# Kernel optimization log

Measured on AMD Instinct MI355X. Metric: run time of the kernel, lower is better.

## Reference

```python
import jax, jax.numpy as jnp
import numpy as np

HIDDEN = 1024
N_HEADS = 16
HEAD_DIM = HIDDEN // N_HEADS  # 64
B, N = 2, 2048
SCALE = HIDDEN ** (-0.5)  # NOTE: original scales by full hidden_size, not head_dim


def setup_inputs() -> dict:
    key = jax.random.key(0)
    k1, k2 = jax.random.split(key)
    hidden_states = jax.random.normal(k1, (B, N, HIDDEN), dtype=jnp.float32)
    attention_mask = jnp.ones((B, N), dtype=jnp.int32)
    # per-head no-bias Linear(hidden -> 3*head_dim), stacked: [h, hidden, 3*head_dim]
    W_qkv = jax.random.normal(k2, (N_HEADS, HIDDEN, 3 * HEAD_DIM), dtype=jnp.float32) * (HIDDEN ** -0.5)
    return {"hidden_states": hidden_states, "attention_mask": attention_mask, "W_qkv": W_qkv}


def reference(hidden_states, attention_mask, W_qkv):
    # qkv: [b, h, n, 3*d]
    qkv = jnp.einsum('bnD,hDe->bhne', hidden_states, W_qkv)
    q, k, v = jnp.split(qkv, 3, axis=-1)  # each [b, h, n, d]
    scores = jnp.einsum('bhid,bhjd->bhij', q, k) * SCALE
    mask = attention_mask[:, None, None, :] == 0  # [b,1,1,n]
    scores = jnp.where(mask, -jnp.inf, scores)
    attn = jax.nn.softmax(scores, axis=-1)
    out = jnp.einsum('bhij,bhjd->bhid', attn, v)  # [b, h, n, d]
    # rearrange 'b h n d -> b n (h d)'
    return jnp.transpose(out, (0, 2, 1, 3)).reshape(out.shape[0], out.shape[2], -1)
```

## Files before the change

kernel.cpp:

```cpp
#include <hip/hip_runtime.h>
#include <hip/hip_bf16.h>


#define NH   16
#define HD   64
#define SEQ  2048
#define HID  1024
#define E3   192
#define QSCALE 0.04508422017f
#define MBIAS  -43.2808512f

typedef __attribute__((ext_vector_type(8))) short short8;
typedef __attribute__((ext_vector_type(4))) float f32x4;
typedef unsigned short ushort_t;

#define MFMA16(a, b, c) __builtin_amdgcn_mfma_f32_16x16x32_bf16((a), (b), (c), 0, 0, 0)

#if __has_builtin(__builtin_amdgcn_exp2f)
#define EXP2(x) __builtin_amdgcn_exp2f(x)
#else
#define EXP2(x) exp2f(x)
#endif

static __device__ __forceinline__ ushort_t f2bf(float x) {
    unsigned u = __builtin_bit_cast(unsigned, x);
    unsigned r = u + 0x7fff + ((u >> 16) & 1);
    return (ushort_t)(r >> 16);
}

static __device__ __forceinline__ unsigned pack_trunc(float hi, float lo) {
#if __has_builtin(__builtin_amdgcn_perm)
    return __builtin_amdgcn_perm(__builtin_bit_cast(unsigned, hi),
                                 __builtin_bit_cast(unsigned, lo), 0x07060302u);
#else
    return (__builtin_bit_cast(unsigned, hi) & 0xffff0000u) |
           (__builtin_bit_cast(unsigned, lo) >> 16);
#endif
}

static __device__ __forceinline__ void load_lds16(const void* g, void* l) {
    __builtin_amdgcn_global_load_lds(
        (__attribute__((address_space(1))) void*)(g),
        (__attribute__((address_space(3))) void*)(l), 16, 0, 0);
}

__global__ void k_detect(const unsigned* __restrict__ X32, int* __restrict__ flagp) {
    __shared__ int cnt;
    if (threadIdx.x == 0) cnt = 0;
    __syncthreads();
    int local = 0;
#pragma unroll
    for (int i = 0; i < 4; ++i) {
        unsigned u = X32[(size_t)(threadIdx.x * 4 + i) * 1973 + 7];
        int b = (u >> 7) & 0xFF;
        if (b >= 0x68 && b <= 0x90) ++local;
    }
    atomicAdd(&cnt, local);
    __syncthreads();
    if (threadIdx.x == 0) *flagp = (cnt < 512) ? 1 : 0;
}

__global__ __launch_bounds__(256) void k_cvt_x(const void* __restrict__ Xv,
                                               ushort_t* __restrict__ Xb,
                                               const int* __restrict__ flagp) {
    const int isf32 = *flagp;
    const size_t base = ((size_t)blockIdx.x * 256 + threadIdx.x) * 16;
    if (isf32) {
        const float* Xf = (const float*)Xv;
        ushort_t tmp[16];
#pragma unroll
        for (int c = 0; c < 4; ++c) {
            float4 v = *(const float4*)(Xf + base + c * 4);
            tmp[c * 4 + 0] = f2bf(v.x); tmp[c * 4 + 1] = f2bf(v.y);
            tmp[c * 4 + 2] = f2bf(v.z); tmp[c * 4 + 3] = f2bf(v.w);
        }
        *(float4*)(Xb + base)     = ((const float4*)tmp)[0];
        *(float4*)(Xb + base + 8) = ((const float4*)tmp)[1];
    } else {
        const ushort_t* Xh = (const ushort_t*)Xv;
        *(float4*)(Xb + base)     = *(const float4*)(Xh + base);
        *(float4*)(Xb + base + 8) = *(const float4*)(Xh + base + 8);
    }
}

__global__ __launch_bounds__(256) void k_cvt_w(const void* __restrict__ Wv,
                                               ushort_t* __restrict__ Wt,
                                               const int* __restrict__ flagp) {
    __shared__ ushort_t tile[64][72];
    const int isf32 = *flagp;
    const int h  = blockIdx.x;
    const int dt = blockIdx.y;
    const int et = blockIdx.z;
    const int D0 = dt * 64, e0 = et * 64;
    const int t  = threadIdx.x;
#pragma unroll
    for (int r = 0; r < 2; ++r) {
        int row = r * 32 + (t >> 3);
        int col = (t & 7) * 8;
        size_t base = ((size_t)(h * HID + D0 + row)) * E3 + e0 + col;
        if (isf32) {
            const float* Wf = (const float*)Wv;
            float4 a = *(const float4*)(Wf + base);
            float4 c = *(const float4*)(Wf + base + 4);
            tile[row][col + 0] = f2bf(a.x); tile[row][col + 1] = f2bf(a.y);
            tile[row][col + 2] = f2bf(a.z); tile[row][col + 3] = f2bf(a.w);
            tile[row][col + 4] = f2bf(c.x); tile[row][col + 5] = f2bf(c.y);
            tile[row][col + 6] = f2bf(c.z); tile[row][col + 7] = f2bf(c.w);
        } else {
            *(float4*)&tile[row][col] = *(const float4*)((const ushort_t*)Wv + base);
        }
    }
    __syncthreads();
#pragma unroll
    for (int r = 0; r < 2; ++r) {
        int erow = r * 32 + (t >> 3);
        int dcol = (t & 7) * 8;
        ushort_t vals[8];
#pragma unroll
        for (int i = 0; i < 8; ++i) vals[i] = tile[dcol + i][erow];
        *(float4*)(Wt + ((size_t)(h * E3 + e0 + erow)) * HID + D0 + dcol) = *(float4*)vals;
    }
}

__global__ __launch_bounds__(256) void k_qkv(const ushort_t* __restrict__ Xb,
                                             const ushort_t* __restrict__ Wt,
                                             ushort_t* __restrict__ Qb,
                                             ushort_t* __restrict__ Kb,
                                             ushort_t* __restrict__ Vtb) {
    __shared__ __align__(16) ushort_t smem[2 * 128 * 64];
    ushort_t* Xl = smem;
    ushort_t* Wl = smem + 128 * 64;

    const int e0 = blockIdx.x * 128;
    const int m0 = blockIdx.y * 128;
    const int b  = m0 >> 11;
    const int n0 = m0 & 2047;
    const int t = threadIdx.x;
    const int w = t >> 6, lane = t & 63, l15 = lane & 15, quad = lane >> 4;
    const int wrow0 = (w & 1) * 64, wcol0 = (w >> 1) * 64;
    const int srow = lane >> 3;
    const int scb  = (lane & 7) ^ srow;

    f32x4 acc[4][4];
#pragma unroll
    for (int i = 0; i < 4; ++i)
#pragma unroll
        for (int j = 0; j < 4; ++j) acc[i][j] = (f32x4){0.f, 0.f, 0.f, 0.f};

    for (int k0 = 0; k0 < HID; k0 += 64) {
        __syncthreads();
#pragma unroll
        for (int cc = 0; cc < 4; ++cc) {
            const int ch  = w * 4 + cc;
            const int row = ch * 8 + srow;
            load_lds16(Xb + (size_t)(m0 + row) * HID + k0 + scb * 8, &Xl[ch * 512]);
            load_lds16(Wt + (size_t)(e0 + row) * HID + k0 + scb * 8, &Wl[ch * 512]);
        }
        __syncthreads();
#pragma unroll
        for (int kh = 0; kh < 2; ++kh) {
            short8 af[4], bfm[4];
#pragma unroll
            for (int i = 0; i < 4; ++i) {
                const int r = wrow0 + i * 16 + l15;
                af[i] = *(const short8*)&Xl[r * 64 + ((kh * 4 + quad) ^ (r & 7)) * 8];
            }
#pragma unroll
            for (int j = 0; j < 4; ++j) {
                const int r = wcol0 + j * 16 + l15;
                bfm[j] = *(const short8*)&Wl[r * 64 + ((kh * 4 + quad) ^ (r & 7)) * 8];
            }
#pragma unroll
            for (int i = 0; i < 4; ++i)
#pragma unroll
                for (int j = 0; j < 4; ++j)
                    acc[i][j] = MFMA16(af[i], bfm[j], acc[i][j]);
        }
    }

    ushort_t* Vbuf = smem;
    __syncthreads();
#pragma unroll
    for (int i = 0; i < 4; ++i) {
#pragma unroll
        for (int j = 0; j < 4; ++j) {
            const int E0v = e0 + wcol0 + j * 16;
            const int hh  = E0v / 192;
            const int r0  = E0v - hh * 192;
            const int bh  = b * NH + hh;
            const int nb  = n0 + wrow0 + i * 16 + quad * 4;
            if (r0 < 64) {
                const int e = r0 + l15;
#pragma unroll
                for (int reg = 0; reg < 4; ++reg)
                    Qb[((size_t)bh * SEQ + nb + reg) * HD + e] = f2bf(acc[i][j][reg] * QSCALE);
            } else if (r0 < 128) {
                const int e = r0 - 64 + l15;
#pragma unroll
                for (int reg = 0; reg < 4; ++reg)
                    Kb[((size_t)bh * SEQ + nb + reg) * HD + e] = f2bf(acc[i][j][reg]);
            } else {
                const int d  = r0 - 128 + l15;
                const int nl = wrow0 + i * 16 + quad * 4;
#pragma unroll
                for (int reg = 0; reg < 4; ++reg)
                    Vbuf[d * 136 + nl + reg] = f2bf(acc[i][j][reg]);
            }
        }
    }
    const int m3 = blockIdx.x % 3;
    if (m3 != 0) {
        __syncthreads();
        const int hv  = (e0 + ((m3 == 1) ? 0 : 64)) / 192;
        const int bhv = b * NH + hv;
        const int dr = t >> 2, part = t & 3;
        size_t dst = ((size_t)bhv * HD + dr) * SEQ + n0 + part * 32;
#pragma unroll
        for (int c = 0; c < 4; ++c) {
            float4 v = *(const float4*)&Vbuf[dr * 136 + part * 32 + c * 8];
            *(float4*)(Vtb + dst + c * 8) = v;
        }
    }
}

__global__ __launch_bounds__(512) void k_attn(const ushort_t* __restrict__ Qb,
                                              const ushort_t* __restrict__ Kb,
                                              const ushort_t* __restrict__ Vtb,
                                              const int* __restrict__ mask,
                                              void* __restrict__ outv,
                                              const int* __restrict__ flagp) {
    __shared__ __align__(16) char smem_raw[59392];
    ushort_t* kvbuf = (ushort_t*)smem_raw;
    ushort_t* Pl    = (ushort_t*)(smem_raw + 32768);
    float*    biasl = (float*)(smem_raw + 51200);

    const int isf32 = *flagp;
    const int q0 = blockIdx.x * 128;
    const int bh = blockIdx.y;
    const int b  = bh >> 4, h = bh & 15;
    const int t  = threadIdx.x;
    const int w  = t >> 6, lane = t & 63, l15 = lane & 15, quad = lane >> 4;
    const int srow = lane >> 3;
    const int scb  = (lane & 7) ^ srow;

    const f32x4 zero4 = {0.f, 0.f, 0.f, 0.f};

    {
        ushort_t* kb = kvbuf;
        ushort_t* vb = kvbuf + 4096;
        const int row = w * 8 + srow;
        load_lds16(Kb  + ((size_t)bh * SEQ + row) * HD + scb * 8, &kb[w * 512]);
        load_lds16(Vtb + ((size_t)bh * HD + row) * SEQ + scb * 8, &vb[w * 512]);
    }

    int lm = 0;
    for (int i = t; i < SEQ; i += 512) {
        int mv = mask[b * SEQ + i];
        biasl[i] = mv ? 0.0f : MBIAS;
        lm |= (mv == 0);
    }
    const int use_bias = __syncthreads_or(lm);

    const int qrow = q0 + w * 16 + l15;
    short8 qa0 = *(const short8*)(Qb + ((size_t)bh * SEQ + qrow) * HD + quad * 8);
    short8 qa1 = *(const short8*)(Qb + ((size_t)bh * SEQ + qrow) * HD + 32 + quad * 8);

    f32x4 o[4];
#pragma unroll
    for (int mt = 0; mt < 4; ++mt) o[mt] = zero4;
    float l_r = 0.f;

    for (int j0 = 0; j0 < SEQ; j0 += 64) {
        const int cur = (j0 >> 6) & 1;
        __syncthreads();
        if (j0 + 64 < SEQ) {
            ushort_t* kb = kvbuf + (1 - cur) * 8192;
            ushort_t* vb = kb + 4096;
            const int row = w * 8 + srow;
            load_lds16(Kb  + ((size_t)bh * SEQ + j0 + 64 + row) * HD + scb * 8, &kb[w * 512]);
            load_lds16(Vtb + ((size_t)bh * HD + row) * SEQ + j0 + 64 + scb * 8, &vb[w * 512]);
        }
        ushort_t* kb = kvbuf + cur * 8192;
        ushort_t* vb = kb + 4096;

        f32x4 s[4];
#pragma unroll
        for (int jt = 0; jt < 4; ++jt) {
            const int rk = jt * 16 + l15;
            short8 kb0 = *(const short8*)&kb[rk * 64 + ((quad)     ^ (rk & 7)) * 8];
            short8 kb1 = *(const short8*)&kb[rk * 64 + ((4 + quad) ^ (rk & 7)) * 8];
            s[jt] = MFMA16(kb0, qa0, zero4);
            s[jt] = MFMA16(kb1, qa1, s[jt]);
        }
        if (use_bias) {
#pragma unroll
            for (int jt = 0; jt < 4; ++jt) {
                float4 bj = *(const float4*)&biasl[j0 + jt * 16 + quad * 4];
#pragma unroll
                for (int reg = 0; reg < 4; ++reg)
                    s[jt][reg] += ((const float*)&bj)[reg];
            }
        }

#pragma unroll
        for (int jt = 0; jt < 4; ++jt) {
            float p0 = EXP2(s[jt][0]);
            float p1 = EXP2(s[jt][1]);
            float p2 = EXP2(s[jt][2]);
            float p3 = EXP2(s[jt][3]);
            l_r += (p0 + p1) + (p2 + p3);
            uint2 u;
            u.x = pack_trunc(p1, p0);
            u.y = pack_trunc(p3, p2);
            *(uint2*)&Pl[(w * 16 + l15) * 72 + jt * 16 + quad * 4] = u;
        }
        short8 pb0 = *(const short8*)&Pl[(w * 16 + l15) * 72 + quad * 8];
        short8 pb1 = *(const short8*)&Pl[(w * 16 + l15) * 72 + 32 + quad * 8];
#pragma unroll
        for (int mt = 0; mt < 4; ++mt) {
            const int rv = mt * 16 + l15;
            short8 va0 = *(const short8*)&vb[rv * 64 + ((quad)     ^ (rv & 7)) * 8];
            short8 va1 = *(const short8*)&vb[rv * 64 + ((4 + quad) ^ (rv & 7)) * 8];
            o[mt] = MFMA16(va0, pb0, o[mt]);
            o[mt] = MFMA16(va1, pb1, o[mt]);
        }
    }

    l_r += __shfl_xor(l_r, 16);
    l_r += __shfl_xor(l_r, 32);
    const float rinv = 1.0f / l_r;

    __syncthreads();
    const int r = t >> 2, part = t & 3;
    if (!isf32) {
        ushort_t* Ol = (ushort_t*)smem_raw;
#pragma unroll
        for (int mt = 0; mt < 4; ++mt) {
            uint2 u;
            u.x = (unsigned)f2bf(o[mt][0] * rinv) | ((unsigned)f2bf(o[mt][1] * rinv) << 16);
            u.y = (unsigned)f2bf(o[mt][2] * rinv) | ((unsigned)f2bf(o[mt][3] * rinv) << 16);
            *(uint2*)&Ol[(w * 16 + l15) * 72 + mt * 16 + quad * 4] = u;
        }
        __syncthreads();
        float4 v0 = *(const float4*)&Ol[r * 72 + part * 16];
        float4 v1 = *(const float4*)&Ol[r * 72 + part * 16 + 8];
        ushort_t* outp = (ushort_t*)outv;
        size_t dst = ((size_t)b * SEQ + q0 + r) * HID + h * HD + part * 16;
        *(float4*)(outp + dst)     = v0;
        *(float4*)(outp + dst + 8) = v1;
    } else {
        float* Olf = (float*)smem_raw;
#pragma unroll
        for (int mt = 0; mt < 4; ++mt)
#pragma unroll
            for (int reg = 0; reg < 4; ++reg)
                Olf[(w * 16 + l15) * 68 + mt * 16 + quad * 4 + reg] = o[mt][reg] * rinv;
        __syncthreads();
        float* outp = (float*)outv;
        size_t dst = ((size_t)b * SEQ + q0 + r) * HID + h * HD + part * 16;
#pragma unroll
        for (int c = 0; c < 4; ++c) {
            float4 v = *(const float4*)&Olf[r * 68 + part * 16 + c * 4];
            *(float4*)(outp + dst + c * 4) = v;
        }
    }
}

extern "C" void kernel_launch(void* const* d_in, const int* in_sizes, int n_in,
                              void* d_out, int out_size, void* d_ws, size_t ws_size,
                              hipStream_t stream) {
    const void* X    = d_in[0];
    const int*  mask = (const int*)d_in[1];
    const void* W    = d_in[2];

    char* ws = (char*)d_ws;
    ushort_t* Qb    = (ushort_t*)(ws);
    ushort_t* Kb    = (ushort_t*)(ws + 8388608);
    ushort_t* Vtb   = (ushort_t*)(ws + 16777216);
    ushort_t* Wtb   = (ushort_t*)(ws + 25165824);
    int*      flagp = (int*)(ws + 31457280);
    ushort_t* Xb    = (ushort_t*)d_out;

    k_detect<<<1, 256, 0, stream>>>((const unsigned*)X, flagp);
    k_cvt_x<<<1024, 256, 0, stream>>>(X, Xb, flagp);
    k_cvt_w<<<dim3(16, 16, 3), 256, 0, stream>>>(W, Wtb, flagp);
    k_qkv<<<dim3(24, 32), 256, 0, stream>>>(Xb, Wtb, Qb, Kb, Vtb);
    k_attn<<<dim3(16, 32), 512, 0, stream>>>(Qb, Kb, Vtb, mask, d_out, flagp);
}
```

Measured before the change: 178.8 us.

## Triple-buffer K/V tiles in attention and fold dtype detection into conversion

The attention kernel moves from double-buffered to triple-buffered K/V LDS tiles. It prefetches two tiles ahead and waits with explicit vmcnt counts before a raw barrier, instead of a full __syncthreads each iteration. This is meant to hide global-to-LDS load latency better, at the cost of more LDS per block, which may lower occupancy. Separately, the standalone dtype-detection launch is removed: each conversion block now samples its own slice of X to decide fp32 vs bf16, and block 0 writes the flag used by later kernels.

```diff
diff --git a/kernel.cpp b/kernel.cpp
--- a/kernel.cpp
+++ b/kernel.cpp
@@ -44,26 +44,22 @@
         (__attribute__((address_space(3))) void*)(l), 16, 0, 0);
 }
 
-__global__ void k_detect(const unsigned* __restrict__ X32, int* __restrict__ flagp) {
+__global__ __launch_bounds__(256) void k_cvt_x(const void* __restrict__ Xv,
+                                               ushort_t* __restrict__ Xb,
+                                               int* __restrict__ flagp) {
     __shared__ int cnt;
     if (threadIdx.x == 0) cnt = 0;
     __syncthreads();
-    int local = 0;
-#pragma unroll
-    for (int i = 0; i < 4; ++i) {
-        unsigned u = X32[(size_t)(threadIdx.x * 4 + i) * 1973 + 7];
-        int b = (u >> 7) & 0xFF;
-        if (b >= 0x68 && b <= 0x90) ++local;
-    }
-    atomicAdd(&cnt, local);
-    __syncthreads();
-    if (threadIdx.x == 0) *flagp = (cnt < 512) ? 1 : 0;
-}
-
-__global__ __launch_bounds__(256) void k_cvt_x(const void* __restrict__ Xv,
-                                               ushort_t* __restrict__ Xb,
-                                               const int* __restrict__ flagp) {
-    const int isf32 = *flagp;
+    const unsigned* X32 = (const unsigned*)Xv;
+    if (threadIdx.x < 64) {
+        unsigned u = X32[(size_t)blockIdx.x * 2048 + threadIdx.x * 32 + 7];
+        int bexp = (u >> 7) & 0xFF;
+        if (bexp >= 0x68 && bexp <= 0x90) atomicAdd(&cnt, 1);
+    }
+    __syncthreads();
+    const int isf32 = (cnt < 32);
+    if (blockIdx.x == 0 && threadIdx.x == 0) *flagp = isf32;
+
     const size_t base = ((size_t)blockIdx.x * 256 + threadIdx.x) * 16;
     if (isf32) {
         const float* Xf = (const float*)Xv;
@@ -229,10 +225,9 @@
                                               const int* __restrict__ mask,
                                               void* __restrict__ outv,
                                               const int* __restrict__ flagp) {
-    __shared__ __align__(16) char smem_raw[59392];
-    ushort_t* kvbuf = (ushort_t*)smem_raw;
-    ushort_t* Pl    = (ushort_t*)(smem_raw + 32768);
-    float*    biasl = (float*)(smem_raw + 51200);
+    __shared__ __align__(16) char smem_raw[75776];
+    ushort_t* Pl    = (ushort_t*)(smem_raw + 49152);
+    float*    biasl = (float*)(smem_raw + 67584);
 
     const int isf32 = *flagp;
     const int q0 = blockIdx.x * 128;
@@ -242,15 +237,16 @@
     const int w  = t >> 6, lane = t & 63, l15 = lane & 15, quad = lane >> 4;
     const int srow = lane >> 3;
     const int scb  = (lane & 7) ^ srow;
+    const int row8 = w * 8 + srow;
 
     const f32x4 zero4 = {0.f, 0.f, 0.f, 0.f};
 
-    {
-        ushort_t* kb = kvbuf;
-        ushort_t* vb = kvbuf + 4096;
-        const int row = w * 8 + srow;
-        load_lds16(Kb  + ((size_t)bh * SEQ + row) * HD + scb * 8, &kb[w * 512]);
-        load_lds16(Vtb + ((size_t)bh * HD + row) * SEQ + scb * 8, &vb[w * 512]);
+#pragma unroll
+    for (int tj = 0; tj < 2; ++tj) {
+        ushort_t* kb = (ushort_t*)(smem_raw + tj * 16384);
+        ushort_t* vb = kb + 4096;
+        load_lds16(Kb  + ((size_t)bh * SEQ + tj * 64 + row8) * HD + scb * 8, &kb[w * 512]);
+        load_lds16(Vtb + ((size_t)bh * HD + row8) * SEQ + tj * 64 + scb * 8, &vb[w * 512]);
     }
 
     int lm = 0;
@@ -259,28 +255,30 @@
         biasl[i] = mv ? 0.0f : MBIAS;
         lm |= (mv == 0);
     }
-    const int use_bias = __syncthreads_or(lm);
-
     const int qrow = q0 + w * 16 + l15;
     short8 qa0 = *(const short8*)(Qb + ((size_t)bh * SEQ + qrow) * HD + quad * 8);
     short8 qa1 = *(const short8*)(Qb + ((size_t)bh * SEQ + qrow) * HD + 32 + quad * 8);
 
+    const int use_bias = __syncthreads_or(lm);
+
     f32x4 o[4];
 #pragma unroll
     for (int mt = 0; mt < 4; ++mt) o[mt] = zero4;
     float l_r = 0.f;
 
     for (int j0 = 0; j0 < SEQ; j0 += 64) {
-        const int cur = (j0 >> 6) & 1;
-        __syncthreads();
-        if (j0 + 64 < SEQ) {
-            ushort_t* kb = kvbuf + (1 - cur) * 8192;
+        const int idx = (j0 >> 6) % 3;
+        if (j0 + 64 < SEQ) { asm volatile("s_waitcnt vmcnt(2)" ::: "memory"); }
+        else               { asm volatile("s_waitcnt vmcnt(0)" ::: "memory"); }
+        __builtin_amdgcn_s_barrier();
+        asm volatile("" ::: "memory");
+        if (j0 + 128 < SEQ) {
+            ushort_t* kb = (ushort_t*)(smem_raw + ((idx + 2) % 3) * 16384);
             ushort_t* vb = kb + 4096;
-            const int row = w * 8 + srow;
-            load_lds16(Kb  + ((size_t)bh * SEQ + j0 + 64 + row) * HD + scb * 8, &kb[w * 512]);
-            load_lds16(Vtb + ((size_t)bh * HD + row) * SEQ + j0 + 64 + scb * 8, &vb[w * 512]);
-        }
-        ushort_t* kb = kvbuf + cur * 8192;
+            load_lds16(Kb  + ((size_t)bh * SEQ + j0 + 128 + row8) * HD + scb * 8, &kb[w * 512]);
+            load_lds16(Vtb + ((size_t)bh * HD + row8) * SEQ + j0 + 128 + scb * 8, &vb[w * 512]);
+        }
+        ushort_t* kb = (ushort_t*)(smem_raw + idx * 16384);
         ushort_t* vb = kb + 4096;
 
         f32x4 s[4];
@@ -381,7 +379,6 @@
     int*      flagp = (int*)(ws + 31457280);
     ushort_t* Xb    = (ushort_t*)d_out;
 
-    k_detect<<<1, 256, 0, stream>>>((const unsigned*)X, flagp);
     k_cvt_x<<<1024, 256, 0, stream>>>(X, Xb, flagp);
     k_cvt_w<<<dim3(16, 16, 3), 256, 0, stream>>>(W, Wtb, flagp);
     k_qkv<<<dim3(24, 32), 256, 0, stream>>>(Xb, Wtb, Qb, Kb, Vtb);
```

Measured after the change: 176.9 us. No clear change (-1.1%).
